# Kernel optimization log

Hardware: AMD Instinct MI355X
Metric: run time of the kernel (lower is better)

The kernel has to match this reference:

```python
import jax, jax.numpy as jnp
import numpy as np

DIM = 512
NUM_CLASSES = 2048
BATCH = 16384


def setup_inputs() -> dict:
    key = jax.random.key(0)
    kx, kc = jax.random.split(key)
    x = jax.random.normal(kx, (BATCH, DIM), dtype=jnp.float32)
    # torch.rand -> uniform [0,1)
    centers = jax.random.uniform(kc, (NUM_CLASSES, DIM), dtype=jnp.float32)
    return {"x": x, "centers": centers}


def reference(x, centers):
    x_sq = jnp.sum(x * x, axis=-1, keepdims=True)            # [B, 1]
    c_sq = jnp.sum(centers * centers, axis=-1)[None, :]      # [1, K]
    cross = jnp.einsum('bd,kd->bk', x, centers)              # [B, K]
    dist_sq = x_sq + c_sq - 2.0 * cross                      # [B, K]
    # responsibilities: stable softmax over -0.5 * dist_sq along classes
    resp = jax.nn.softmax(-0.5 * dist_sq, axis=-1)
    return resp
```

## Files before the change

kernel.cpp:

```cpp
#include <hip/hip_runtime.h>

#define BATCH 16384
#define DIM   512
#define NCLS  2048

typedef _Float16 half8 __attribute__((ext_vector_type(8)));
typedef float    floatx4 __attribute__((ext_vector_type(4)));

#define GLB(p) ((const __attribute__((address_space(1))) void*)(p))
#define LDSP(p) ((__attribute__((address_space(3))) void*)(p))

__global__ __launch_bounds__(256) void cvt_kernel(const float* __restrict__ src,
                                                  _Float16* __restrict__ dst) {
    size_t i = ((size_t)blockIdx.x * 256 + threadIdx.x) * 8;
    float4 a = *reinterpret_cast<const float4*>(src + i);
    float4 b = *reinterpret_cast<const float4*>(src + i + 4);
    half8 h;
    h[0] = (_Float16)a.x; h[1] = (_Float16)a.y; h[2] = (_Float16)a.z; h[3] = (_Float16)a.w;
    h[4] = (_Float16)b.x; h[5] = (_Float16)b.y; h[6] = (_Float16)b.z; h[7] = (_Float16)b.w;
    *reinterpret_cast<half8*>(dst + i) = h;
}

__global__ __launch_bounds__(64) void csq_kernel(const float* __restrict__ c,
                                                 float* __restrict__ hcsq) {
    int k = blockIdx.x, t = threadIdx.x;
    const float4* p = reinterpret_cast<const float4*>(c + (size_t)k * DIM);
    float s = 0.f;
    #pragma unroll
    for (int j = 0; j < 2; ++j) {
        float4 v = p[t + j * 64];
        s += v.x * v.x + v.y * v.y + v.z * v.z + v.w * v.w;
    }
    #pragma unroll
    for (int o = 32; o; o >>= 1) s += __shfl_xor(s, o);
    if (t == 0) hcsq[k] = 0.5f * s;
}

__global__ __launch_bounds__(256) void gemm_kernel(const _Float16* __restrict__ A,
                                                   const _Float16* __restrict__ B,
                                                   float* __restrict__ C) {
    __shared__ __align__(16) _Float16 As[128 * 32];
    __shared__ __align__(16) _Float16 Bs[128 * 32];

    const int bid  = blockIdx.x;
    const int rowB = (bid >> 4) << 7;
    const int colB = (bid & 15) << 7;
    const int tid  = threadIdx.x;
    const int lane = tid & 63;
    const int wave = tid >> 6;
    const int wr   = wave >> 1, wc = wave & 1;

    const _Float16* agp = A + (size_t)(rowB + wave * 32 + (lane >> 2)) * DIM + (lane & 3) * 8;
    const _Float16* bgp = B + (size_t)(colB + wave * 32 + (lane >> 2)) * DIM + (lane & 3) * 8;
    _Float16* alp = &As[(wave * 32) * 32];
    _Float16* blp = &Bs[(wave * 32) * 32];

    const int fko  = (lane >> 4) * 8;
    const int arow = wr * 64 + (lane & 15);
    const int brow = wc * 64 + (lane & 15);

    floatx4 acc[4][4] = {};

    for (int kk = 0; kk < DIM / 32; ++kk) {
        __builtin_amdgcn_global_load_lds(GLB(agp),            LDSP(alp),           16, 0, 0);
        __builtin_amdgcn_global_load_lds(GLB(agp + 16 * DIM), LDSP(alp + 16 * 32), 16, 0, 0);
        __builtin_amdgcn_global_load_lds(GLB(bgp),            LDSP(blp),           16, 0, 0);
        __builtin_amdgcn_global_load_lds(GLB(bgp + 16 * DIM), LDSP(blp + 16 * 32), 16, 0, 0);
        agp += 32;
        bgp += 32;
        __syncthreads();

        half8 af[4], bf[4];
        #pragma unroll
        for (int m = 0; m < 4; ++m)
            af[m] = *reinterpret_cast<const half8*>(&As[(arow + m * 16) * 32 + fko]);
        #pragma unroll
        for (int n = 0; n < 4; ++n)
            bf[n] = *reinterpret_cast<const half8*>(&Bs[(brow + n * 16) * 32 + fko]);

        #pragma unroll
        for (int m = 0; m < 4; ++m)
            #pragma unroll
            for (int n = 0; n < 4; ++n)
                acc[m][n] = __builtin_amdgcn_mfma_f32_16x16x32_f16(af[m], bf[n], acc[m][n], 0, 0, 0);

        __syncthreads();
    }

    const int crow = rowB + wr * 64 + ((lane >> 4) << 2);
    const int ccol = colB + wc * 64 + (lane & 15);
    #pragma unroll
    for (int m = 0; m < 4; ++m)
        #pragma unroll
        for (int n = 0; n < 4; ++n)
            #pragma unroll
            for (int j = 0; j < 4; ++j)
                C[(size_t)(crow + m * 16 + j) * NCLS + ccol + n * 16] = acc[m][n][j];
}

__global__ __launch_bounds__(256) void softmax_kernel(float* __restrict__ O,
                                                      const float* __restrict__ hcsq) {
    const int row  = blockIdx.x;
    const int tid  = threadIdx.x;
    const int lane = tid & 63, wave = tid >> 6;

    float4* Orow = reinterpret_cast<float4*>(O + (size_t)row * NCLS);
    const float4* Q = reinterpret_cast<const float4*>(hcsq);

    float4 v0 = Orow[tid];
    float4 v1 = Orow[tid + 256];
    float4 q0 = Q[tid];
    float4 q1 = Q[tid + 256];
    v0.x -= q0.x; v0.y -= q0.y; v0.z -= q0.z; v0.w -= q0.w;
    v1.x -= q1.x; v1.y -= q1.y; v1.z -= q1.z; v1.w -= q1.w;

    float m = fmaxf(fmaxf(fmaxf(v0.x, v0.y), fmaxf(v0.z, v0.w)),
                    fmaxf(fmaxf(v1.x, v1.y), fmaxf(v1.z, v1.w)));
    #pragma unroll
    for (int o = 32; o; o >>= 1) m = fmaxf(m, __shfl_xor(m, o));
    __shared__ float redm[4];
    __shared__ float reds[4];
    if (lane == 0) redm[wave] = m;
    __syncthreads();
    m = fmaxf(fmaxf(redm[0], redm[1]), fmaxf(redm[2], redm[3]));

    v0.x = __expf(v0.x - m); v0.y = __expf(v0.y - m); v0.z = __expf(v0.z - m); v0.w = __expf(v0.w - m);
    v1.x = __expf(v1.x - m); v1.y = __expf(v1.y - m); v1.z = __expf(v1.z - m); v1.w = __expf(v1.w - m);
    float s = v0.x + v0.y + v0.z + v0.w + v1.x + v1.y + v1.z + v1.w;
    #pragma unroll
    for (int o = 32; o; o >>= 1) s += __shfl_xor(s, o);
    if (lane == 0) reds[wave] = s;
    __syncthreads();
    s = reds[0] + reds[1] + reds[2] + reds[3];

    float inv = 1.0f / s;
    v0.x *= inv; v0.y *= inv; v0.z *= inv; v0.w *= inv;
    v1.x *= inv; v1.y *= inv; v1.z *= inv; v1.w *= inv;
    Orow[tid]       = v0;
    Orow[tid + 256] = v1;
}

extern "C" void kernel_launch(void* const* d_in, const int* in_sizes, int n_in,
                              void* d_out, int out_size, void* d_ws, size_t ws_size,
                              hipStream_t stream) {
    const float* x       = (const float*)d_in[0];
    const float* centers = (const float*)d_in[1];
    float* out = (float*)d_out;

    _Float16* xh = (_Float16*)d_ws;
    _Float16* ch = xh + (size_t)BATCH * DIM;
    float* hcsq  = (float*)(ch + (size_t)NCLS * DIM);

    hipLaunchKernelGGL(cvt_kernel, dim3(BATCH * DIM / (8 * 256)), dim3(256), 0, stream, x, xh);
    hipLaunchKernelGGL(cvt_kernel, dim3(NCLS * DIM / (8 * 256)), dim3(256), 0, stream, centers, ch);
    hipLaunchKernelGGL(csq_kernel, dim3(NCLS), dim3(64), 0, stream, centers, hcsq);
    hipLaunchKernelGGL(gemm_kernel, dim3((BATCH / 128) * (NCLS / 128)), dim3(256), 0, stream,
                       xh, ch, out);
    hipLaunchKernelGGL(softmax_kernel, dim3(BATCH), dim3(256), 0, stream, out, hcsq);
}
```

Measured before the change: 119.0 us.

## Fuse x conversion, GEMM and softmax into one row-block kernel

```diff
diff --git a/kernel.cpp b/kernel.cpp
--- a/kernel.cpp
+++ b/kernel.cpp
@@ -36,108 +36,165 @@
     if (t == 0) hcsq[k] = 0.5f * s;
 }
 
-__global__ __launch_bounds__(256) void gemm_kernel(const _Float16* __restrict__ A,
-                                                   const _Float16* __restrict__ B,
-                                                   float* __restrict__ C) {
-    __shared__ __align__(16) _Float16 As[128 * 32];
-    __shared__ __align__(16) _Float16 Bs[128 * 32];
-
-    const int bid  = blockIdx.x;
-    const int rowB = (bid >> 4) << 7;
-    const int colB = (bid & 15) << 7;
+__global__ __launch_bounds__(512, 2) void fused_kernel(
+    const float* __restrict__ X,
+    const _Float16* __restrict__ Bh,
+    const float* __restrict__ hcsq,
+    float* __restrict__ O)
+{
+    __shared__ __align__(16) _Float16 As[32 * 512];
+    __shared__ __align__(16) _Float16 Bs[2][256 * 64];
+    __shared__ float redm[4][32];
+    __shared__ float reds[4][32];
+
     const int tid  = threadIdx.x;
     const int lane = tid & 63;
     const int wave = tid >> 6;
-    const int wr   = wave >> 1, wc = wave & 1;
-
-    const _Float16* agp = A + (size_t)(rowB + wave * 32 + (lane >> 2)) * DIM + (lane & 3) * 8;
-    const _Float16* bgp = B + (size_t)(colB + wave * 32 + (lane >> 2)) * DIM + (lane & 3) * 8;
-    _Float16* alp = &As[(wave * 32) * 32];
-    _Float16* blp = &Bs[(wave * 32) * 32];
-
-    const int fko  = (lane >> 4) * 8;
-    const int arow = wr * 64 + (lane & 15);
-    const int brow = wc * 64 + (lane & 15);
-
-    floatx4 acc[4][4] = {};
-
-    for (int kk = 0; kk < DIM / 32; ++kk) {
-        __builtin_amdgcn_global_load_lds(GLB(agp),            LDSP(alp),           16, 0, 0);
-        __builtin_amdgcn_global_load_lds(GLB(agp + 16 * DIM), LDSP(alp + 16 * 32), 16, 0, 0);
-        __builtin_amdgcn_global_load_lds(GLB(bgp),            LDSP(blp),           16, 0, 0);
-        __builtin_amdgcn_global_load_lds(GLB(bgp + 16 * DIM), LDSP(blp + 16 * 32), 16, 0, 0);
-        agp += 32;
-        bgp += 32;
-        __syncthreads();
-
-        half8 af[4], bf[4];
-        #pragma unroll
-        for (int m = 0; m < 4; ++m)
-            af[m] = *reinterpret_cast<const half8*>(&As[(arow + m * 16) * 32 + fko]);
-        #pragma unroll
-        for (int n = 0; n < 4; ++n)
-            bf[n] = *reinterpret_cast<const half8*>(&Bs[(brow + n * 16) * 32 + fko]);
-
-        #pragma unroll
-        for (int m = 0; m < 4; ++m)
-            #pragma unroll
-            for (int n = 0; n < 4; ++n)
-                acc[m][n] = __builtin_amdgcn_mfma_f32_16x16x32_f16(af[m], bf[n], acc[m][n], 0, 0, 0);
-
-        __syncthreads();
-    }
-
-    const int crow = rowB + wr * 64 + ((lane >> 4) << 2);
-    const int ccol = colB + wc * 64 + (lane & 15);
-    #pragma unroll
-    for (int m = 0; m < 4; ++m)
-        #pragma unroll
-        for (int n = 0; n < 4; ++n)
+    const int rt   = wave & 1;
+    const int cg   = wave >> 1;
+    const int rowB = blockIdx.x * 32;
+
+    #pragma unroll
+    for (int i = 0; i < 4; ++i) {
+        int G = i * 512 + tid;
+        int row = G >> 6, g = G & 63;
+        const float* src = X + (size_t)(rowB + row) * DIM + g * 8;
+        float4 a = *reinterpret_cast<const float4*>(src);
+        float4 b = *reinterpret_cast<const float4*>(src + 4);
+        half8 h;
+        h[0] = (_Float16)a.x; h[1] = (_Float16)a.y; h[2] = (_Float16)a.z; h[3] = (_Float16)a.w;
+        h[4] = (_Float16)b.x; h[5] = (_Float16)b.y; h[6] = (_Float16)b.z; h[7] = (_Float16)b.w;
+        int dg = row * 64 + (g ^ (row & 7));
+        *reinterpret_cast<half8*>(&As[dg * 8]) = h;
+    }
+
+    auto stage_b = [&](int c2, int k2, int buf) {
+        const int lcol = lane >> 3;
+        const int sw   = (lane & 7) ^ lcol;
+        #pragma unroll
+        for (int i = 0; i < 4; ++i) {
+            const int col = wave * 32 + i * 8 + lcol;
+            const _Float16* src = Bh + (size_t)(c2 * 256 + col) * DIM + k2 * 64 + sw * 8;
+            _Float16* dst = &Bs[buf][(wave * 4 + i) * 512];
+            __builtin_amdgcn_global_load_lds(GLB(src), LDSP(dst), 16, 0, 0);
+        }
+    };
+
+    stage_b(0, 0, 0);
+    __syncthreads();
+
+    floatx4 acc[4] = {};
+    floatx4 logv[8][4];
+    float hc[4];
+
+    #pragma unroll
+    for (int chunk = 0; chunk < 8; ++chunk) {
+        #pragma unroll
+        for (int ct = 0; ct < 4; ++ct)
+            hc[ct] = hcsq[chunk * 256 + cg * 64 + ct * 16 + (lane & 15)];
+
+        #pragma unroll
+        for (int ks = 0; ks < 8; ++ks) {
+            const int t = chunk * 8 + ks;
+            if (t < 63) {
+                const int tn = t + 1;
+                stage_b(tn >> 3, tn & 7, tn & 1);
+            }
+            const int buf = t & 1;
+            #pragma unroll
+            for (int k2 = 0; k2 < 2; ++k2) {
+                const int arow = rt * 16 + (lane & 15);
+                const int ag   = ks * 8 + k2 * 4 + (lane >> 4);
+                half8 af = *reinterpret_cast<const half8*>(
+                    &As[arow * 512 + (ag ^ (lane & 7)) * 8]);
+                #pragma unroll
+                for (int ct = 0; ct < 4; ++ct) {
+                    const int bcol = cg * 64 + ct * 16 + (lane & 15);
+                    const int bg   = k2 * 4 + (lane >> 4);
+                    half8 bf = *reinterpret_cast<const half8*>(
+                        &Bs[buf][bcol * 64 + (bg ^ (lane & 7)) * 8]);
+                    acc[ct] = __builtin_amdgcn_mfma_f32_16x16x32_f16(af, bf, acc[ct], 0, 0, 0);
+                }
+            }
+            __syncthreads();
+        }
+        #pragma unroll
+        for (int ct = 0; ct < 4; ++ct) {
+            floatx4 v = acc[ct];
+            v[0] -= hc[ct]; v[1] -= hc[ct]; v[2] -= hc[ct]; v[3] -= hc[ct];
+            logv[chunk][ct] = v;
+            acc[ct] = (floatx4){0.f, 0.f, 0.f, 0.f};
+        }
+    }
+
+    float mj[4] = {-1e30f, -1e30f, -1e30f, -1e30f};
+    #pragma unroll
+    for (int c = 0; c < 8; ++c)
+        #pragma unroll
+        for (int ct = 0; ct < 4; ++ct)
             #pragma unroll
             for (int j = 0; j < 4; ++j)
-                C[(size_t)(crow + m * 16 + j) * NCLS + ccol + n * 16] = acc[m][n][j];
-}
-
-__global__ __launch_bounds__(256) void softmax_kernel(float* __restrict__ O,
-                                                      const float* __restrict__ hcsq) {
-    const int row  = blockIdx.x;
-    const int tid  = threadIdx.x;
-    const int lane = tid & 63, wave = tid >> 6;
-
-    float4* Orow = reinterpret_cast<float4*>(O + (size_t)row * NCLS);
-    const float4* Q = reinterpret_cast<const float4*>(hcsq);
-
-    float4 v0 = Orow[tid];
-    float4 v1 = Orow[tid + 256];
-    float4 q0 = Q[tid];
-    float4 q1 = Q[tid + 256];
-    v0.x -= q0.x; v0.y -= q0.y; v0.z -= q0.z; v0.w -= q0.w;
-    v1.x -= q1.x; v1.y -= q1.y; v1.z -= q1.z; v1.w -= q1.w;
-
-    float m = fmaxf(fmaxf(fmaxf(v0.x, v0.y), fmaxf(v0.z, v0.w)),
-                    fmaxf(fmaxf(v1.x, v1.y), fmaxf(v1.z, v1.w)));
-    #pragma unroll
-    for (int o = 32; o; o >>= 1) m = fmaxf(m, __shfl_xor(m, o));
-    __shared__ float redm[4];
-    __shared__ float reds[4];
-    if (lane == 0) redm[wave] = m;
+                mj[j] = fmaxf(mj[j], logv[c][ct][j]);
+    #pragma unroll
+    for (int off = 8; off >= 1; off >>= 1)
+        #pragma unroll
+        for (int j = 0; j < 4; ++j)
+            mj[j] = fmaxf(mj[j], __shfl_xor(mj[j], off));
+    if ((lane & 15) == 0) {
+        #pragma unroll
+        for (int j = 0; j < 4; ++j)
+            redm[cg][rt * 16 + (lane >> 4) * 4 + j] = mj[j];
+    }
     __syncthreads();
-    m = fmaxf(fmaxf(redm[0], redm[1]), fmaxf(redm[2], redm[3]));
-
-    v0.x = __expf(v0.x - m); v0.y = __expf(v0.y - m); v0.z = __expf(v0.z - m); v0.w = __expf(v0.w - m);
-    v1.x = __expf(v1.x - m); v1.y = __expf(v1.y - m); v1.z = __expf(v1.z - m); v1.w = __expf(v1.w - m);
-    float s = v0.x + v0.y + v0.z + v0.w + v1.x + v1.y + v1.z + v1.w;
-    #pragma unroll
-    for (int o = 32; o; o >>= 1) s += __shfl_xor(s, o);
-    if (lane == 0) reds[wave] = s;
+
+    float M[4];
+    #pragma unroll
+    for (int j = 0; j < 4; ++j) {
+        const int row = rt * 16 + (lane >> 4) * 4 + j;
+        M[j] = fmaxf(fmaxf(redm[0][row], redm[1][row]),
+                     fmaxf(redm[2][row], redm[3][row]));
+    }
+
+    float sj[4] = {0.f, 0.f, 0.f, 0.f};
+    #pragma unroll
+    for (int c = 0; c < 8; ++c)
+        #pragma unroll
+        for (int ct = 0; ct < 4; ++ct)
+            #pragma unroll
+            for (int j = 0; j < 4; ++j) {
+                float e = __expf(logv[c][ct][j] - M[j]);
+                logv[c][ct][j] = e;
+                sj[j] += e;
+            }
+    #pragma unroll
+    for (int off = 8; off >= 1; off >>= 1)
+        #pragma unroll
+        for (int j = 0; j < 4; ++j)
+            sj[j] += __shfl_xor(sj[j], off);
+    if ((lane & 15) == 0) {
+        #pragma unroll
+        for (int j = 0; j < 4; ++j)
+            reds[cg][rt * 16 + (lane >> 4) * 4 + j] = sj[j];
+    }
     __syncthreads();
-    s = reds[0] + reds[1] + reds[2] + reds[3];
-
-    float inv = 1.0f / s;
-    v0.x *= inv; v0.y *= inv; v0.z *= inv; v0.w *= inv;
-    v1.x *= inv; v1.y *= inv; v1.z *= inv; v1.w *= inv;
-    Orow[tid]       = v0;
-    Orow[tid + 256] = v1;
+
+    float inv[4];
+    #pragma unroll
+    for (int j = 0; j < 4; ++j) {
+        const int row = rt * 16 + (lane >> 4) * 4 + j;
+        inv[j] = 1.0f / (reds[0][row] + reds[1][row] + reds[2][row] + reds[3][row]);
+    }
+
+    #pragma unroll
+    for (int c = 0; c < 8; ++c)
+        #pragma unroll
+        for (int ct = 0; ct < 4; ++ct) {
+            const int col = c * 256 + cg * 64 + ct * 16 + (lane & 15);
+            float* op = O + (size_t)(rowB + rt * 16 + (lane >> 4) * 4) * NCLS + col;
+            #pragma unroll
+            for (int j = 0; j < 4; ++j)
+                op[(size_t)j * NCLS] = logv[c][ct][j] * inv[j];
+        }
 }
 
 extern "C" void kernel_launch(void* const* d_in, const int* in_sizes, int n_in,
@@ -147,14 +204,12 @@
     const float* centers = (const float*)d_in[1];
     float* out = (float*)d_out;
 
-    _Float16* xh = (_Float16*)d_ws;
-    _Float16* ch = xh + (size_t)BATCH * DIM;
+    _Float16* ch = (_Float16*)d_ws;
     float* hcsq  = (float*)(ch + (size_t)NCLS * DIM);
 
-    hipLaunchKernelGGL(cvt_kernel, dim3(BATCH * DIM / (8 * 256)), dim3(256), 0, stream, x, xh);
-    hipLaunchKernelGGL(cvt_kernel, dim3(NCLS * DIM / (8 * 256)), dim3(256), 0, stream, centers, ch);
+    hipLaunchKernelGGL(cvt_kernel, dim3(NCLS * DIM / (8 * 256)), dim3(256), 0, stream,
+                       centers, ch);
     hipLaunchKernelGGL(csq_kernel, dim3(NCLS), dim3(64), 0, stream, centers, hcsq);
-    hipLaunchKernelGGL(gemm_kernel, dim3((BATCH / 128) * (NCLS / 128)), dim3(256), 0, stream,
-                       xh, ch, out);
-    hipLaunchKernelGGL(softmax_kernel, dim3(BATCH), dim3(256), 0, stream, out, hcsq);
-}
+    hipLaunchKernelGGL(fused_kernel, dim3(BATCH / 32), dim3(512), 0, stream,
+                       x, ch, hcsq, out);
+}
```

Result: slower. 131.3 us, median of 2 (+10.3%).
